# Optimization experiments

Hardware: AMD Instinct MI355X
Metric: run time of the kernel (lower is better)

The kernel has to match this reference:

```python
import jax, jax.numpy as jnp
import numpy as np

N_NODES = 100000
N_EDGES = 2500000
IN_CH = 32
HID = 16
OUT_CH = 32


def setup_inputs() -> dict:
    key = jax.random.key(0)
    ks = jax.random.split(key, 10)
    x = jax.random.normal(ks[0], (N_NODES, IN_CH), dtype=jnp.float32)
    edge_index = jax.random.randint(ks[1], (2, N_EDGES), 0, N_NODES, dtype=jnp.int64)
    # conv1 MLP: Linear(in,16) -> ReLU -> Linear(16,out)
    W1 = jax.random.normal(ks[2], (IN_CH, HID), dtype=jnp.float32) / np.sqrt(IN_CH)
    b1 = jnp.zeros((HID,), dtype=jnp.float32)
    W2 = jax.random.normal(ks[3], (HID, OUT_CH), dtype=jnp.float32) / np.sqrt(HID)
    b2 = jnp.zeros((OUT_CH,), dtype=jnp.float32)
    # conv2 MLP: Linear(out,16) -> ReLU -> Linear(16,out)
    W3 = jax.random.normal(ks[4], (OUT_CH, HID), dtype=jnp.float32) / np.sqrt(OUT_CH)
    b3 = jnp.zeros((HID,), dtype=jnp.float32)
    W4 = jax.random.normal(ks[5], (HID, OUT_CH), dtype=jnp.float32) / np.sqrt(HID)
    b4 = jnp.zeros((OUT_CH,), dtype=jnp.float32)
    return {"x": x, "edge_index": edge_index, "W1": W1, "b1": b1, "W2": W2,
            "b2": b2, "W3": W3, "b3": b3, "W4": W4, "b4": b4}


def _gin_conv(x, src, dst, W_a, b_a, W_b, b_b):
    # GINConv (eps=0): nn((1+eps)*x + sum_{j in N(i)} x_j)
    agg = jax.ops.segment_sum(x[src], dst, num_segments=x.shape[0])  # [N, d]
    h = x + agg
    h = jnp.maximum(h @ W_a + b_a, 0.0)  # Linear -> ReLU
    return h @ W_b + b_b                 # Linear


def reference(x, edge_index, W1, b1, W2, b2, W3, b3, W4, b4):
    src, dst = edge_index[0], edge_index[1]
    h = _gin_conv(x, src, dst, W1, b1, W2, b2)
    h = jnp.maximum(h, 0.0)  # F.relu between convs
    out = _gin_conv(h, src, dst, W3, b3, W4, b4)
    return out
```

## Files before the change

kernel.cpp:

```cpp
#include <hip/hip_runtime.h>

typedef unsigned short ushort_t;
typedef unsigned int uint_t;

#define BKT_SHIFT 8
#define BKT_NODES 256
#define NBKT_MAX 400
#define EPB 8192
#define SCOL_CAP 8192
#define NPB 16
#define SCOL_N 768

__device__ __forceinline__ ushort_t f2bf(float f) {
    unsigned u = __float_as_uint(f);
    unsigned r = (u + 0x7FFFu + ((u >> 16) & 1u)) >> 16;
    return (ushort_t)r;
}

__global__ void to_bf16(const float4* __restrict__ in, ushort_t* __restrict__ out, int n4) {
    int i = blockIdx.x * blockDim.x + threadIdx.x;
    if (i < n4) {
        float4 v = in[i];
        out[i * 4 + 0] = f2bf(v.x);
        out[i * 4 + 1] = f2bf(v.y);
        out[i * 4 + 2] = f2bf(v.z);
        out[i * 4 + 3] = f2bf(v.w);
    }
}


__global__ void histA(const int* __restrict__ dst, int* __restrict__ hist,
                      int E, int NBKT) {
    __shared__ int lcnt[NBKT_MAX];
    int t = threadIdx.x, blk = blockIdx.x;
    for (int b = t; b < NBKT; b += 512) lcnt[b] = 0;
    __syncthreads();
    int e0 = blk * EPB;
    #pragma unroll
    for (int i = 0; i < 16; ++i) {
        int e = e0 + i * 512 + t;
        if (e < E) atomicAdd(&lcnt[dst[e] >> BKT_SHIFT], 1);
    }
    __syncthreads();
    for (int b = t; b < NBKT; b += 512) hist[blk * NBKT + b] = lcnt[b];
}

__global__ void colscan(int* __restrict__ hist, int* __restrict__ T,
                        int NBLK, int NBKT) {
    __shared__ int lds[256];
    int b = blockIdx.x, t = threadIdx.x;
    int j0 = t * 4;
    int v0 = (j0 + 0 < NBLK) ? hist[(j0 + 0) * NBKT + b] : 0;
    int v1 = (j0 + 1 < NBLK) ? hist[(j0 + 1) * NBKT + b] : 0;
    int v2 = (j0 + 2 < NBLK) ? hist[(j0 + 2) * NBKT + b] : 0;
    int v3 = (j0 + 3 < NBLK) ? hist[(j0 + 3) * NBKT + b] : 0;
    lds[t] = v0 + v1 + v2 + v3;
    __syncthreads();
    for (int off = 1; off < 256; off <<= 1) {
        int add = (t >= off) ? lds[t - off] : 0;
        __syncthreads();
        lds[t] += add;
        __syncthreads();
    }
    int p = (t == 0) ? 0 : lds[t - 1];
    if (j0 + 0 < NBLK) hist[(j0 + 0) * NBKT + b] = p;  p += v0;
    if (j0 + 1 < NBLK) hist[(j0 + 1) * NBKT + b] = p;  p += v1;
    if (j0 + 2 < NBLK) hist[(j0 + 2) * NBKT + b] = p;  p += v2;
    if (j0 + 3 < NBLK) hist[(j0 + 3) * NBKT + b] = p;
    if (t == 255) T[b] = lds[255];
}

__global__ void scan_small(const int* __restrict__ in, int* __restrict__ out,
                           int M, int E) {
    __shared__ int lds[1024];
    int t = threadIdx.x;
    int base = t * 4;
    int v0 = (base + 0 < M) ? in[base + 0] : 0;
    int v1 = (base + 1 < M) ? in[base + 1] : 0;
    int v2 = (base + 2 < M) ? in[base + 2] : 0;
    int v3 = (base + 3 < M) ? in[base + 3] : 0;
    lds[t] = v0 + v1 + v2 + v3;
    __syncthreads();
    for (int off = 1; off < 1024; off <<= 1) {
        int add = (t >= off) ? lds[t - off] : 0;
        __syncthreads();
        lds[t] += add;
        __syncthreads();
    }
    int p = (t == 0) ? 0 : lds[t - 1];
    if (base + 0 < M) out[base + 0] = p;  p += v0;
    if (base + 1 < M) out[base + 1] = p;  p += v1;
    if (base + 2 < M) out[base + 2] = p;  p += v2;
    if (base + 3 < M) out[base + 3] = p;
    if (t == 0) out[M] = E;
}

__global__ void scatter_kernel(const int* __restrict__ src, const int* __restrict__ dst,
                               const int* __restrict__ hist, const int* __restrict__ Tscan,
                               int* __restrict__ staged, int E, int NBKT) {
    __shared__ int lbase[NBKT_MAX];
    __shared__ int lcur[NBKT_MAX];
    int t = threadIdx.x, blk = blockIdx.x;
    for (int b = t; b < NBKT; b += 512) {
        lbase[b] = hist[blk * NBKT + b] + Tscan[b];
        lcur[b] = 0;
    }
    __syncthreads();
    int e0 = blk * EPB;
    #pragma unroll
    for (int i = 0; i < 16; ++i) {
        int e = e0 + i * 512 + t;
        if (e < E) {
            int d = dst[e], s = src[e];
            int b = d >> BKT_SHIFT;
            int r = atomicAdd(&lcur[b], 1);
            staged[lbase[b] + r] = ((d & (BKT_NODES - 1)) << 24) | s;
        }
    }
}

__global__ void fine_fill(const int* __restrict__ staged, const int* __restrict__ Tscan,
                          int* __restrict__ rp, int* __restrict__ col,
                          int N, int E, int NBKT) {
    __shared__ int scnt[256];
    __shared__ int srel[256];
    __shared__ int scur[256];
    __shared__ int scol[SCOL_CAP];
    int b = blockIdx.x, t = threadIdx.x;
    int n0 = b << BKT_SHIFT;
    int nn = min(BKT_NODES, N - n0);
    int e0 = Tscan[b];
    int e1 = Tscan[b + 1];
    int m = e1 - e0;

    scnt[t] = 0; scur[t] = 0;
    __syncthreads();
    for (int i = t; i < m; i += 256) {
        int dl = ((unsigned)staged[e0 + i]) >> 24;
        atomicAdd(&scnt[dl], 1);
    }
    __syncthreads();
    int inc_in = scnt[t];
    for (int off = 1; off < 256; off <<= 1) {
        int add = (t >= off) ? scnt[t - off] : 0;
        __syncthreads();
        scnt[t] += add;
        __syncthreads();
    }
    int excl = scnt[t] - inc_in;
    srel[t] = excl;
    if (t < nn) rp[n0 + t] = e0 + excl;
    if (b == NBKT - 1 && t == 0) rp[N] = E;
    __syncthreads();

    if (m <= SCOL_CAP) {
        for (int i = t; i < m; i += 256) {
            int v = staged[e0 + i];
            int dl = ((unsigned)v) >> 24;
            int p = srel[dl] + atomicAdd(&scur[dl], 1);
            scol[p] = v & 0xFFFFFF;
        }
        __syncthreads();
        for (int i = t; i < m; i += 256) col[e0 + i] = scol[i];
    } else {
        for (int i = t; i < m; i += 256) {
            int v = staged[e0 + i];
            int dl = ((unsigned)v) >> 24;
            int p = srel[dl] + atomicAdd(&scur[dl], 1);
            col[e0 + p] = v & 0xFFFFFF;
        }
    }
}


template <bool RELU_OUT, bool OUT_BF16>
__global__ void agg_mlp(const ushort_t* __restrict__ xin, const int* __restrict__ rp,
                        const int* __restrict__ col,
                        const float* __restrict__ Wa, const float* __restrict__ ba,
                        const float* __restrict__ Wb, const float* __restrict__ bb,
                        void* __restrict__ outv, int N) {
    __shared__ float sWa[32 * 16];
    __shared__ float sWb[16 * 32];
    __shared__ float sba[16], sbb[32];
    __shared__ float sv[NPB][32];
    __shared__ float st1[NPB][16];
    __shared__ int scol[SCOL_N];

    int t = threadIdx.x;
    sWa[t] = Wa[t];  sWa[t + 256] = Wa[t + 256];
    sWb[t] = Wb[t];  sWb[t + 256] = Wb[t + 256];
    if (t < 16) sba[t] = ba[t];
    if (t < 32) sbb[t] = bb[t];

    int base = blockIdx.x * NPB;
    int kb = rp[base];
    int kt = rp[min(base + NPB, N)];
    int tot = kt - kb;
    bool ovf = (tot > SCOL_N);
    if (!ovf) {
        for (int i = t; i < tot; i += 256)
            scol[i] = __builtin_nontemporal_load(col + kb + i);
    }
    __syncthreads();

    int ln = t >> 4;
    int sl = t & 15;
    int n  = base + ln;
    bool act = (n < N);
    const uint_t* x32 = (const uint_t*)xin;

    if (act) {
        uint_t us = x32[(size_t)n * 16 + sl];
        float vx = __uint_as_float(us << 16);
        float vy = __uint_as_float(us & 0xFFFF0000u);
        int ks = rp[n], ke = rp[n + 1];
        if (!ovf) {
            int k = ks - kb, kend = ke - kb;
            for (; k + 8 <= kend; k += 8) {
                int s0 = scol[k + 0], s1 = scol[k + 1], s2 = scol[k + 2], s3 = scol[k + 3];
                int s4 = scol[k + 4], s5 = scol[k + 5], s6 = scol[k + 6], s7 = scol[k + 7];
                uint_t u0 = x32[(size_t)s0 * 16 + sl];
                uint_t u1 = x32[(size_t)s1 * 16 + sl];
                uint_t u2 = x32[(size_t)s2 * 16 + sl];
                uint_t u3 = x32[(size_t)s3 * 16 + sl];
                uint_t u4 = x32[(size_t)s4 * 16 + sl];
                uint_t u5 = x32[(size_t)s5 * 16 + sl];
                uint_t u6 = x32[(size_t)s6 * 16 + sl];
                uint_t u7 = x32[(size_t)s7 * 16 + sl];
                vx += ((__uint_as_float(u0 << 16) + __uint_as_float(u1 << 16))
                     + (__uint_as_float(u2 << 16) + __uint_as_float(u3 << 16)))
                    + ((__uint_as_float(u4 << 16) + __uint_as_float(u5 << 16))
                     + (__uint_as_float(u6 << 16) + __uint_as_float(u7 << 16)));
                vy += ((__uint_as_float(u0 & 0xFFFF0000u) + __uint_as_float(u1 & 0xFFFF0000u))
                     + (__uint_as_float(u2 & 0xFFFF0000u) + __uint_as_float(u3 & 0xFFFF0000u)))
                    + ((__uint_as_float(u4 & 0xFFFF0000u) + __uint_as_float(u5 & 0xFFFF0000u))
                     + (__uint_as_float(u6 & 0xFFFF0000u) + __uint_as_float(u7 & 0xFFFF0000u)));
            }
            for (; k < kend; ++k) {
                uint_t u0 = x32[(size_t)scol[k] * 16 + sl];
                vx += __uint_as_float(u0 << 16);
                vy += __uint_as_float(u0 & 0xFFFF0000u);
            }
        } else {
            for (int k = ks; k < ke; ++k) {
                uint_t u0 = x32[(size_t)col[k] * 16 + sl];
                vx += __uint_as_float(u0 << 16);
                vy += __uint_as_float(u0 & 0xFFFF0000u);
            }
        }
        sv[ln][2 * sl]     = vx;
        sv[ln][2 * sl + 1] = vy;
    }
    __syncthreads();

    if (act) {
        float h = sba[sl];
        #pragma unroll
        for (int cc = 0; cc < 32; ++cc) h += sv[ln][cc] * sWa[cc * 16 + sl];
        st1[ln][sl] = fmaxf(h, 0.f);
    }
    __syncthreads();

    if (act) {
        int c0 = 2 * sl;
        float a0 = sbb[c0], a1 = sbb[c0 + 1];
        #pragma unroll
        for (int j = 0; j < 16; ++j) {
            float hj = st1[ln][j];
            a0 += hj * sWb[j * 32 + c0];
            a1 += hj * sWb[j * 32 + c0 + 1];
        }
        if (RELU_OUT) { a0 = fmaxf(a0, 0.f); a1 = fmaxf(a1, 0.f); }
        if (OUT_BF16) {
            uint_t p = (uint_t)f2bf(a0) | ((uint_t)f2bf(a1) << 16);
            __builtin_nontemporal_store(p, (uint_t*)outv + (size_t)n * 16 + sl);
        } else {
            float* o = (float*)outv + (size_t)n * 32 + 2 * sl;
            __builtin_nontemporal_store(a0, o);
            __builtin_nontemporal_store(a1, o + 1);
        }
    }
}


extern "C" void kernel_launch(void* const* d_in, const int* in_sizes, int n_in,
                              void* d_out, int out_size, void* d_ws, size_t ws_size,
                              hipStream_t stream) {
    const float* x  = (const float*)d_in[0];
    const int*   ei = (const int*)d_in[1];
    const float* W1 = (const float*)d_in[2];
    const float* b1 = (const float*)d_in[3];
    const float* W2 = (const float*)d_in[4];
    const float* b2 = (const float*)d_in[5];
    const float* W3 = (const float*)d_in[6];
    const float* b3 = (const float*)d_in[7];
    const float* W4 = (const float*)d_in[8];
    const float* b4 = (const float*)d_in[9];

    const int N = in_sizes[0] / 32;
    const int E = in_sizes[1] / 2;
    const int* src = ei;
    const int* dst = ei + E;

    const int NBKT = (N + BKT_NODES - 1) >> BKT_SHIFT;
    const int NBLK = (E + EPB - 1) / EPB;

    char* ws = (char*)d_ws;
    size_t o = 0;
    auto alloc = [&](size_t bytes) -> char* {
        o = (o + 255) & ~(size_t)255;
        char* r = ws + o;
        o += bytes;
        return r;
    };
    int*      hist   = (int*)     alloc(4 * (size_t)NBLK * NBKT);
    int*      T      = (int*)     alloc(4 * (size_t)NBKT);
    int*      Tscan  = (int*)     alloc(4 * (size_t)(NBKT + 1));
    int*      staged = (int*)     alloc(4 * (size_t)E);
    int*      rp     = (int*)     alloc(4 * (size_t)(N + 1));
    int*      col    = (int*)     alloc(4 * (size_t)E);
    ushort_t* xb     = (ushort_t*)alloc(2 * (size_t)N * 32);
    ushort_t* hb     = (ushort_t*)alloc(2 * (size_t)N * 32);

    int n4 = N * 32 / 4;
    to_bf16<<<(n4 + 255) / 256, 256, 0, stream>>>((const float4*)x, xb, n4);

    histA<<<NBLK, 512, 0, stream>>>(dst, hist, E, NBKT);
    colscan<<<NBKT, 256, 0, stream>>>(hist, T, NBLK, NBKT);
    scan_small<<<1, 1024, 0, stream>>>(T, Tscan, NBKT, E);
    scatter_kernel<<<NBLK, 512, 0, stream>>>(src, dst, hist, Tscan, staged, E, NBKT);
    fine_fill<<<NBKT, 256, 0, stream>>>(staged, Tscan, rp, col, N, E, NBKT);

    agg_mlp<true,  true ><<<(N + NPB - 1) / NPB, 256, 0, stream>>>(xb, rp, col,
                                                                   W1, b1, W2, b2, hb, N);
    agg_mlp<false, false><<<(N + NPB - 1) / NPB, 256, 0, stream>>>(hb, rp, col,
                                                                   W3, b3, W4, b4, d_out, N);
}
```

Baseline: 213.0 us.

## Widen gather to 8-byte lanes and quarter-sort CSR neighbors by source range

The aggregation kernel now has 8 lanes per node, each loading a uint2 (four bf16 values), and handles 32 nodes per block with padded shared arrays to avoid bank conflicts. fine_fill now sorts each node's neighbor list into four source-ID quartiles. This groups gathers within a node toward nearby memory regions, which should improve cache locality. The changes aim to cut the number of load instructions and raise L2 hit rate during the gather, at the cost of extra shared memory and counting work in fine_fill.

```diff
diff --git a/kernel.cpp b/kernel.cpp
--- a/kernel.cpp
+++ b/kernel.cpp
@@ -8,14 +8,16 @@
 #define NBKT_MAX 400
 #define EPB 8192
 #define SCOL_CAP 8192
-#define NPB 16
-#define SCOL_N 768
+#define NPB 32
+#define SCOL_N 1536
 
 __device__ __forceinline__ ushort_t f2bf(float f) {
     unsigned u = __float_as_uint(f);
     unsigned r = (u + 0x7FFFu + ((u >> 16) & 1u)) >> 16;
     return (ushort_t)r;
 }
+__device__ __forceinline__ float bflo(uint_t u) { return __uint_as_float(u << 16); }
+__device__ __forceinline__ float bfhi(uint_t u) { return __uint_as_float(u & 0xFFFF0000u); }
 
 __global__ void to_bf16(const float4* __restrict__ in, ushort_t* __restrict__ out, int n4) {
     int i = blockIdx.x * blockDim.x + threadIdx.x;
@@ -121,10 +123,11 @@
 
 __global__ void fine_fill(const int* __restrict__ staged, const int* __restrict__ Tscan,
                           int* __restrict__ rp, int* __restrict__ col,
-                          int N, int E, int NBKT) {
-    __shared__ int scnt[256];
-    __shared__ int srel[256];
-    __shared__ int scur[256];
+                          int N, int E, int NBKT, int q1, int q2, int q3) {
+    __shared__ int scnt[1024];
+    __shared__ int srel[1024];
+    __shared__ int scur[1024];
+    __shared__ int swsum[256];
     __shared__ int scol[SCOL_CAP];
     int b = blockIdx.x, t = threadIdx.x;
     int n0 = b << BKT_SHIFT;
@@ -133,22 +136,33 @@
     int e1 = Tscan[b + 1];
     int m = e1 - e0;
 
-    scnt[t] = 0; scur[t] = 0;
+    #pragma unroll
+    for (int j = 0; j < 4; ++j) { scnt[t * 4 + j] = 0; scur[t * 4 + j] = 0; }
     __syncthreads();
     for (int i = t; i < m; i += 256) {
-        int dl = ((unsigned)staged[e0 + i]) >> 24;
-        atomicAdd(&scnt[dl], 1);
-    }
-    __syncthreads();
-    int inc_in = scnt[t];
+        int v = staged[e0 + i];
+        int dl = ((unsigned)v) >> 24;
+        int s = v & 0xFFFFFF;
+        int q = (s >= q2) ? ((s >= q3) ? 3 : 2) : ((s >= q1) ? 1 : 0);
+        atomicAdd(&scnt[dl * 4 + q], 1);
+    }
+    __syncthreads();
+    int c0 = scnt[t * 4 + 0], c1 = scnt[t * 4 + 1];
+    int c2 = scnt[t * 4 + 2], c3 = scnt[t * 4 + 3];
+    int tot = c0 + c1 + c2 + c3;
+    swsum[t] = tot;
+    __syncthreads();
     for (int off = 1; off < 256; off <<= 1) {
-        int add = (t >= off) ? scnt[t - off] : 0;
-        __syncthreads();
-        scnt[t] += add;
-        __syncthreads();
-    }
-    int excl = scnt[t] - inc_in;
-    srel[t] = excl;
+        int add = (t >= off) ? swsum[t - off] : 0;
+        __syncthreads();
+        swsum[t] += add;
+        __syncthreads();
+    }
+    int excl = swsum[t] - tot;
+    srel[t * 4 + 0] = excl;
+    srel[t * 4 + 1] = excl + c0;
+    srel[t * 4 + 2] = excl + c0 + c1;
+    srel[t * 4 + 3] = excl + c0 + c1 + c2;
     if (t < nn) rp[n0 + t] = e0 + excl;
     if (b == NBKT - 1 && t == 0) rp[N] = E;
     __syncthreads();
@@ -157,8 +171,10 @@
         for (int i = t; i < m; i += 256) {
             int v = staged[e0 + i];
             int dl = ((unsigned)v) >> 24;
-            int p = srel[dl] + atomicAdd(&scur[dl], 1);
-            scol[p] = v & 0xFFFFFF;
+            int s = v & 0xFFFFFF;
+            int q = (s >= q2) ? ((s >= q3) ? 3 : 2) : ((s >= q1) ? 1 : 0);
+            int p = srel[dl * 4 + q] + atomicAdd(&scur[dl * 4 + q], 1);
+            scol[p] = s;
         }
         __syncthreads();
         for (int i = t; i < m; i += 256) col[e0 + i] = scol[i];
@@ -166,8 +182,10 @@
         for (int i = t; i < m; i += 256) {
             int v = staged[e0 + i];
             int dl = ((unsigned)v) >> 24;
-            int p = srel[dl] + atomicAdd(&scur[dl], 1);
-            col[e0 + p] = v & 0xFFFFFF;
+            int s = v & 0xFFFFFF;
+            int q = (s >= q2) ? ((s >= q3) ? 3 : 2) : ((s >= q1) ? 1 : 0);
+            int p = srel[dl * 4 + q] + atomicAdd(&scur[dl * 4 + q], 1);
+            col[e0 + p] = s;
         }
     }
 }
@@ -182,8 +200,8 @@
     __shared__ float sWa[32 * 16];
     __shared__ float sWb[16 * 32];
     __shared__ float sba[16], sbb[32];
-    __shared__ float sv[NPB][32];
-    __shared__ float st1[NPB][16];
+    __shared__ float sv[NPB * 33];
+    __shared__ float st1[NPB * 17];
     __shared__ int scol[SCOL_N];
 
     int t = threadIdx.x;
@@ -203,81 +221,94 @@
     }
     __syncthreads();
 
-    int ln = t >> 4;
-    int sl = t & 15;
+    int ln = t >> 3;
+    int sl = t & 7;
     int n  = base + ln;
     bool act = (n < N);
-    const uint_t* x32 = (const uint_t*)xin;
+    const uint2* x2 = (const uint2*)xin;
 
     if (act) {
-        uint_t us = x32[(size_t)n * 16 + sl];
-        float vx = __uint_as_float(us << 16);
-        float vy = __uint_as_float(us & 0xFFFF0000u);
+        uint2 us = x2[(size_t)n * 8 + sl];
+        float v0 = bflo(us.x), v1 = bfhi(us.x), v2 = bflo(us.y), v3 = bfhi(us.y);
         int ks = rp[n], ke = rp[n + 1];
         if (!ovf) {
             int k = ks - kb, kend = ke - kb;
             for (; k + 8 <= kend; k += 8) {
                 int s0 = scol[k + 0], s1 = scol[k + 1], s2 = scol[k + 2], s3 = scol[k + 3];
                 int s4 = scol[k + 4], s5 = scol[k + 5], s6 = scol[k + 6], s7 = scol[k + 7];
-                uint_t u0 = x32[(size_t)s0 * 16 + sl];
-                uint_t u1 = x32[(size_t)s1 * 16 + sl];
-                uint_t u2 = x32[(size_t)s2 * 16 + sl];
-                uint_t u3 = x32[(size_t)s3 * 16 + sl];
-                uint_t u4 = x32[(size_t)s4 * 16 + sl];
-                uint_t u5 = x32[(size_t)s5 * 16 + sl];
-                uint_t u6 = x32[(size_t)s6 * 16 + sl];
-                uint_t u7 = x32[(size_t)s7 * 16 + sl];
-                vx += ((__uint_as_float(u0 << 16) + __uint_as_float(u1 << 16))
-                     + (__uint_as_float(u2 << 16) + __uint_as_float(u3 << 16)))
-                    + ((__uint_as_float(u4 << 16) + __uint_as_float(u5 << 16))
-                     + (__uint_as_float(u6 << 16) + __uint_as_float(u7 << 16)));
-                vy += ((__uint_as_float(u0 & 0xFFFF0000u) + __uint_as_float(u1 & 0xFFFF0000u))
-                     + (__uint_as_float(u2 & 0xFFFF0000u) + __uint_as_float(u3 & 0xFFFF0000u)))
-                    + ((__uint_as_float(u4 & 0xFFFF0000u) + __uint_as_float(u5 & 0xFFFF0000u))
-                     + (__uint_as_float(u6 & 0xFFFF0000u) + __uint_as_float(u7 & 0xFFFF0000u)));
+                uint2 u0 = x2[(size_t)s0 * 8 + sl];
+                uint2 u1 = x2[(size_t)s1 * 8 + sl];
+                uint2 u2 = x2[(size_t)s2 * 8 + sl];
+                uint2 u3 = x2[(size_t)s3 * 8 + sl];
+                uint2 u4 = x2[(size_t)s4 * 8 + sl];
+                uint2 u5 = x2[(size_t)s5 * 8 + sl];
+                uint2 u6 = x2[(size_t)s6 * 8 + sl];
+                uint2 u7 = x2[(size_t)s7 * 8 + sl];
+                v0 += ((bflo(u0.x) + bflo(u1.x)) + (bflo(u2.x) + bflo(u3.x)))
+                    + ((bflo(u4.x) + bflo(u5.x)) + (bflo(u6.x) + bflo(u7.x)));
+                v1 += ((bfhi(u0.x) + bfhi(u1.x)) + (bfhi(u2.x) + bfhi(u3.x)))
+                    + ((bfhi(u4.x) + bfhi(u5.x)) + (bfhi(u6.x) + bfhi(u7.x)));
+                v2 += ((bflo(u0.y) + bflo(u1.y)) + (bflo(u2.y) + bflo(u3.y)))
+                    + ((bflo(u4.y) + bflo(u5.y)) + (bflo(u6.y) + bflo(u7.y)));
+                v3 += ((bfhi(u0.y) + bfhi(u1.y)) + (bfhi(u2.y) + bfhi(u3.y)))
+                    + ((bfhi(u4.y) + bfhi(u5.y)) + (bfhi(u6.y) + bfhi(u7.y)));
             }
             for (; k < kend; ++k) {
-                uint_t u0 = x32[(size_t)scol[k] * 16 + sl];
-                vx += __uint_as_float(u0 << 16);
-                vy += __uint_as_float(u0 & 0xFFFF0000u);
+                uint2 u = x2[(size_t)scol[k] * 8 + sl];
+                v0 += bflo(u.x); v1 += bfhi(u.x); v2 += bflo(u.y); v3 += bfhi(u.y);
             }
         } else {
             for (int k = ks; k < ke; ++k) {
-                uint_t u0 = x32[(size_t)col[k] * 16 + sl];
-                vx += __uint_as_float(u0 << 16);
-                vy += __uint_as_float(u0 & 0xFFFF0000u);
+                uint2 u = x2[(size_t)col[k] * 8 + sl];
+                v0 += bflo(u.x); v1 += bfhi(u.x); v2 += bflo(u.y); v3 += bfhi(u.y);
             }
         }
-        sv[ln][2 * sl]     = vx;
-        sv[ln][2 * sl + 1] = vy;
+        int c0 = sl * 4;
+        sv[ln * 33 + c0 + 0] = v0; sv[ln * 33 + c0 + 1] = v1;
+        sv[ln * 33 + c0 + 2] = v2; sv[ln * 33 + c0 + 3] = v3;
     }
     __syncthreads();
 
     if (act) {
-        float h = sba[sl];
+        float ha = sba[sl], hb = sba[sl + 8];
         #pragma unroll
-        for (int cc = 0; cc < 32; ++cc) h += sv[ln][cc] * sWa[cc * 16 + sl];
-        st1[ln][sl] = fmaxf(h, 0.f);
+        for (int cc = 0; cc < 32; ++cc) {
+            float vc = sv[ln * 33 + cc];
+            ha += vc * sWa[cc * 16 + sl];
+            hb += vc * sWa[cc * 16 + sl + 8];
+        }
+        st1[ln * 17 + sl]     = fmaxf(ha, 0.f);
+        st1[ln * 17 + sl + 8] = fmaxf(hb, 0.f);
     }
     __syncthreads();
 
     if (act) {
-        int c0 = 2 * sl;
-        float a0 = sbb[c0], a1 = sbb[c0 + 1];
+        int c0 = sl * 4;
+        float a0 = sbb[c0], a1 = sbb[c0 + 1], a2 = sbb[c0 + 2], a3 = sbb[c0 + 3];
         #pragma unroll
         for (int j = 0; j < 16; ++j) {
-            float hj = st1[ln][j];
+            float hj = st1[ln * 17 + j];
             a0 += hj * sWb[j * 32 + c0];
             a1 += hj * sWb[j * 32 + c0 + 1];
-        }
-        if (RELU_OUT) { a0 = fmaxf(a0, 0.f); a1 = fmaxf(a1, 0.f); }
+            a2 += hj * sWb[j * 32 + c0 + 2];
+            a3 += hj * sWb[j * 32 + c0 + 3];
+        }
+        if (RELU_OUT) {
+            a0 = fmaxf(a0, 0.f); a1 = fmaxf(a1, 0.f);
+            a2 = fmaxf(a2, 0.f); a3 = fmaxf(a3, 0.f);
+        }
         if (OUT_BF16) {
-            uint_t p = (uint_t)f2bf(a0) | ((uint_t)f2bf(a1) << 16);
-            __builtin_nontemporal_store(p, (uint_t*)outv + (size_t)n * 16 + sl);
+            uint_t p0 = (uint_t)f2bf(a0) | ((uint_t)f2bf(a1) << 16);
+            uint_t p1 = (uint_t)f2bf(a2) | ((uint_t)f2bf(a3) << 16);
+            uint_t* o = (uint_t*)outv + (size_t)n * 16 + sl * 2;
+            __builtin_nontemporal_store(p0, o);
+            __builtin_nontemporal_store(p1, o + 1);
         } else {
-            float* o = (float*)outv + (size_t)n * 32 + 2 * sl;
+            float* o = (float*)outv + (size_t)n * 32 + c0;
             __builtin_nontemporal_store(a0, o);
             __builtin_nontemporal_store(a1, o + 1);
+            __builtin_nontemporal_store(a2, o + 2);
+            __builtin_nontemporal_store(a3, o + 3);
         }
     }
 }
@@ -329,7 +360,8 @@
     colscan<<<NBKT, 256, 0, stream>>>(hist, T, NBLK, NBKT);
     scan_small<<<1, 1024, 0, stream>>>(T, Tscan, NBKT, E);
     scatter_kernel<<<NBLK, 512, 0, stream>>>(src, dst, hist, Tscan, staged, E, NBKT);
-    fine_fill<<<NBKT, 256, 0, stream>>>(staged, Tscan, rp, col, N, E, NBKT);
+    int q1 = N / 4, q2 = N / 2, q3 = (3 * N) / 4;
+    fine_fill<<<NBKT, 256, 0, stream>>>(staged, Tscan, rp, col, N, E, NBKT, q1, q2, q3);
 
     agg_mlp<true,  true ><<<(N + NPB - 1) / NPB, 256, 0, stream>>>(xb, rp, col,
                                                                    W1, b1, W2, b2, hb, N);
```

Measured after the change: 206.0 us. -3.3%, faster.
